# Kernel tuning notes

Measured on AMD Instinct MI355X. Metric: run time of the kernel, lower is better.

The kernel has to match this reference:

```python
import jax, jax.numpy as jnp
import numpy as np

K = 32  # neighbors per query point


def _gather_points(x, idx):
    # x: [B, N, D], idx: [B, M, k] -> [B, M, k, D]
    B, M, k = idx.shape
    D = x.shape[-1]
    flat = jnp.take_along_axis(x, idx.reshape(B, M * k, 1), axis=1)
    return flat.reshape(B, M, k, D)


def setup_inputs() -> dict:
    key = jax.random.key(0)
    k1, k2, k3, k4, k5 = jax.random.split(key, 5)
    B, N, M, Cin = 16, 4096, 1024, 64
    pos = jax.random.normal(k1, (B, N, 3), dtype=jnp.float32)
    features = jax.random.normal(k2, (B, N, Cin), dtype=jnp.float32)
    idx = jax.random.randint(k3, (B, M), 0, N, dtype=jnp.int64)
    # 1x1 conv2d MLP params: (Cin+3) -> 64 -> 128 (use_xyz adds 3 channels)
    W1 = jax.random.normal(k4, (Cin + 3, 64), dtype=jnp.float32) * (1.0 / np.sqrt(Cin + 3))
    b1 = jnp.zeros((64,), dtype=jnp.float32)
    W2 = jax.random.normal(k5, (64, 128), dtype=jnp.float32) * (1.0 / np.sqrt(64))
    b2 = jnp.zeros((128,), dtype=jnp.float32)
    return {"pos": pos, "features": features, "W1": W1, "b1": b1,
            "W2": W2, "b2": b2, "idx": idx}


def reference(pos, features, W1, b1, W2, b2, idx):
    # pos: [B,N,3], features: [B,N,C], idx: [B,M] query-point indices
    pos_q = jnp.take_along_axis(pos, idx[..., None], axis=1)  # [B,M,3]
    # squared-distance knn: [B,M,N]
    d2 = (jnp.sum(pos_q ** 2, -1, keepdims=True)
          + jnp.sum(pos ** 2, -1)[:, None, :]
          - 2.0 * jnp.einsum("bmd,bnd->bmn", pos_q, pos))
    _, nn_idx = jax.lax.top_k(-d2, K)  # [B,M,K] nearest neighbors
    grouped_pos = _gather_points(pos, nn_idx)          # [B,M,K,3]
    grouped_feat = _gather_points(features, nn_idx)    # [B,M,K,C]
    rel = grouped_pos - pos_q[:, :, None, :]           # recenter groups
    x = jnp.concatenate([rel, grouped_feat], axis=-1)  # [B,M,K,C+3] (use_xyz)
    # 1x1 conv2d MLP == per-point linear + ReLU on channel dim
    h = jax.nn.relu(jnp.einsum("bmkc,cd->bmkd", x, W1) + b1)
    h = jax.nn.relu(jnp.einsum("bmkc,cd->bmkd", h, W2) + b2)
    out = jnp.max(h, axis=-2)  # max over K neighbors -> [B,M,128]
    return (pos_q, out)
```

## Files before the change

### kernel.cpp

```cpp
#include <hip/hip_runtime.h>

#define NPTS  4096
#define MQ    1024
#define BATCH 16
#define KNN   32
#define CIN   64
#define H1D   64
#define H2D   128

typedef _Float16 half8 __attribute__((ext_vector_type(8)));
typedef float    floatx4 __attribute__((ext_vector_type(4)));

#define WS_NN_BYTES ((size_t)BATCH * MQ * KNN * 4)
#define W1F_HALVES  (3 * 4 * 64 * 8)
#define W2F_HALVES  (2 * 8 * 64 * 8)
#define WS_P4_OFF   (WS_NN_BYTES + (W1F_HALVES + W2F_HALVES) * 2)

__global__ __launch_bounds__(256) void wprep_kernel(
    const float* __restrict__ W1, const float* __restrict__ W2,
    const float* __restrict__ pos,
    _Float16* __restrict__ wout, float4* __restrict__ pos4)
{
    const int gid = blockIdx.x * 256 + threadIdx.x;
    if (gid < 768) {
        const int s = gid;
        const int kc = s >> 8, nt = (s >> 6) & 3, lane = s & 63;
        const int col = lane & 15, quad = lane >> 4;
        half8 ph;
#pragma unroll
        for (int j = 0; j < 8; ++j) {
            const int k = kc * 32 + quad * 8 + j;
            ph[j] = (k < 67) ? (_Float16)W1[k * H1D + nt * 16 + col] : (_Float16)0.0f;
        }
        *(half8*)(wout + (size_t)s * 8) = ph;
    } else if (gid < 1792) {
        const int s2 = gid - 768;
        const int kc2 = s2 >> 9, nt2 = (s2 >> 6) & 7, lane = s2 & 63;
        const int col = lane & 15, quad = lane >> 4;
        half8 ph;
#pragma unroll
        for (int j = 0; j < 8; ++j) {
            const int k = kc2 * 32 + quad * 8 + j;
            ph[j] = (_Float16)W2[k * H2D + nt2 * 16 + col];
        }
        *(half8*)(wout + (size_t)W1F_HALVES + (size_t)s2 * 8) = ph;
    } else {
        const int p = gid - 1792;
        if (p < BATCH * NPTS) {
            const float px = pos[p * 3 + 0], py = pos[p * 3 + 1], pz = pos[p * 3 + 2];
            float4 v;
            v.x = px; v.y = py; v.z = pz;
            v.w = __fadd_rn(__fadd_rn(__fmul_rn(px, px), __fmul_rn(py, py)),
                            __fmul_rn(pz, pz));
            pos4[p] = v;
        }
    }
}

__global__ __launch_bounds__(256, 4) void knn_kernel(
    const float4* __restrict__ pos4, const int* __restrict__ idx,
    float* __restrict__ pos_q, int* __restrict__ nn)
{
    const int bid = blockIdx.x;
    const int b   = bid >> 10;
    const int m   = bid & (MQ - 1);
    const int t   = threadIdx.x;
    const int wv  = t >> 6, lane = t & 63;

    __shared__ unsigned int hist[2048];
    __shared__ unsigned int wsum[4];
    __shared__ unsigned int sc[8];
    __shared__ unsigned int ckey[64];
    __shared__ int          cidx[64];
    __shared__ int          outidx[KNN];

    const float4* pb4 = pos4 + (size_t)b * NPTS;
    const int qn = idx[(size_t)b * MQ + m];
    const float4 qv = pb4[qn];
    const float qq = qv.w;

#pragma unroll
    for (int j = 0; j < 8; ++j) hist[t + 256 * j] = 0u;
    __syncthreads();

    float4 p[16];
#pragma unroll
    for (int i = 0; i < 16; ++i) p[i] = pb4[i * 256 + t];

    unsigned int k[16];
#pragma unroll
    for (int i = 0; i < 16; ++i) {
        const float qp = __fadd_rn(__fadd_rn(__fmul_rn(qv.x, p[i].x), __fmul_rn(qv.y, p[i].y)),
                                   __fmul_rn(qv.z, p[i].z));
        const float d2 = __fsub_rn(__fadd_rn(qq, p[i].w), __fmul_rn(2.0f, qp));
        unsigned int u = __float_as_uint(d2);
        u = (u & 0x80000000u) ? ~u : (u | 0x80000000u);
        k[i] = u;
        atomicAdd(&hist[u >> 21], 1u);
    }
    __syncthreads();

    unsigned int prefix = 0u, rank = KNN - 1;
    int shift = 21, bcnt;
    for (int level = 0; level < 3; ++level) {
        const int nb = (level < 2) ? 11 : 10;
        const int g  = (1 << nb) >> 8;
        unsigned int cnt[8];
        unsigned int s = 0;
        for (int j = 0; j < g; ++j) { cnt[j] = hist[t * g + j]; s += cnt[j]; }
        unsigned int v = s;
#pragma unroll
        for (int off = 1; off < 64; off <<= 1) {
            const unsigned int o = __shfl_up(v, off);
            if (lane >= off) v += o;
        }
        if (lane == 63) wsum[wv] = v;
        __syncthreads();
        unsigned int woff = 0;
        for (int i = 0; i < wv; ++i) woff += wsum[i];
        const unsigned int incl = woff + v, excl = incl - s;
        if (rank >= excl && rank < incl) {
            unsigned int e = excl;
            for (int j = 0; j < g; ++j) {
                if (rank < e + cnt[j]) {
                    sc[0] = (prefix << nb) | (unsigned int)(t * g + j);
                    sc[1] = rank - e;
                    sc[2] = cnt[j];
                    break;
                }
                e += cnt[j];
            }
        }
        __syncthreads();
        prefix = sc[0];
        rank   = sc[1];
        bcnt   = (int)sc[2];
        if (level == 2 || bcnt <= 64) break;

        const int nshift = (level == 0) ? 10 : 0;
        const int nnb    = (level == 0) ? 11 : 10;
        const unsigned int nmask = (1u << nnb) - 1u;
        __syncthreads();
#pragma unroll
        for (int j = 0; j < 8; ++j) hist[t + 256 * j] = 0u;
        __syncthreads();
#pragma unroll
        for (int i = 0; i < 16; ++i) {
            const unsigned int u = k[i];
            if ((u >> (nshift + nnb)) == prefix)
                atomicAdd(&hist[(u >> nshift) & nmask], 1u);
        }
        shift = nshift;
        __syncthreads();
    }

    if (t == 0) { sc[3] = 0u; sc[4] = 0u; }
    __syncthreads();
#pragma unroll
    for (int i = 0; i < 16; ++i) {
        const unsigned int u = k[i];
        const unsigned int hp = (shift == 0) ? u : (u >> shift);
        if (hp < prefix) {
            outidx[atomicAdd(&sc[3], 1u)] = i * 256 + t;
        } else if (hp == prefix) {
            const unsigned int slot = atomicAdd(&sc[4], 1u);
            if (slot < 64u) { ckey[slot] = u; cidx[slot] = i * 256 + t; }
        }
    }
    __syncthreads();
    const int defcnt  = (int)sc[3];
    const int candcnt = min((int)sc[4], 64);

    if (wv == 0) {
        const unsigned int k_l = (lane < candcnt) ? ckey[lane] : 0xFFFFFFFFu;
        const int          i_l = (lane < candcnt) ? cidx[lane] : 0x7FFFFFFF;
        int rk = 0;
        for (int j = 0; j < candcnt; ++j) {
            const unsigned int kj = __shfl(k_l, j);
            const int          ij = __shfl(i_l, j);
            if (kj < k_l || (kj == k_l && ij < i_l)) ++rk;
        }
        if (lane < candcnt && rk <= (int)rank) outidx[defcnt + rk] = i_l;
    }
    __syncthreads();
    if (t < KNN) nn[(size_t)bid * KNN + t] = outidx[t];
    if (t == 0) {
        pos_q[(size_t)bid * 3 + 0] = qv.x;
        pos_q[(size_t)bid * 3 + 1] = qv.y;
        pos_q[(size_t)bid * 3 + 2] = qv.z;
    }
}

__global__ __launch_bounds__(256, 4) void mlp_kernel(
    const float4* __restrict__ pos4, const float* __restrict__ feat,
    const float* __restrict__ b1, const float* __restrict__ b2,
    const float* __restrict__ pos_q, const int* __restrict__ nn,
    const _Float16* __restrict__ wf, float* __restrict__ out)
{
    __shared__ _Float16 sh[4 * 3072];
    const int t = threadIdx.x;
    const int w = t >> 6, lane = t & 63;
    const int col = lane & 15, quad = lane >> 4;
    const int q = blockIdx.x * 4 + w;
    const int b = q >> 10;
    const int wbase = w * 3072;

    {
        const int r = t >> 1, h = t & 1;
        const int kk = r & 31;
        const int n = nn[(size_t)q * KNN + kk];
        const float4 pv = pos4[(size_t)b * NPTS + n];
        const float4* f4 = (const float4*)(feat + ((size_t)b * NPTS + n) * CIN);
        const int mt = kk >> 4, lrow = kk & 15;
        if (h == 0) {
            float4 ff[12];
#pragma unroll
            for (int ii = 0; ii < 12; ++ii) ff[ii] = f4[ii];
            float rel[3];
            rel[0] = pv.x - pos_q[(size_t)q * 3 + 0];
            rel[1] = pv.y - pos_q[(size_t)q * 3 + 1];
            rel[2] = pv.z - pos_q[(size_t)q * 3 + 2];
#pragma unroll
            for (int ci = 0; ci < 6; ++ci) {
                half8 ph;
#pragma unroll
                for (int jj = 0; jj < 8; ++jj) {
                    const int c = ci * 8 + jj;
                    float v;
                    if (c < 3) v = rel[c];
                    else {
                        const int fc = c - 3;
                        const float4 vv = ff[fc >> 2];
                        v = ((fc & 3) == 0) ? vv.x : ((fc & 3) == 1) ? vv.y
                          : ((fc & 3) == 2) ? vv.z : vv.w;
                    }
                    ph[jj] = (_Float16)v;
                }
                const int kc = ci >> 2, qd = ci & 3;
                *(half8*)&sh[wbase + ((kc * 2 + mt) * 64 + qd * 16 + lrow) * 8] = ph;
            }
        } else {
            float4 ff[5];
#pragma unroll
            for (int ii = 0; ii < 5; ++ii) ff[ii] = f4[11 + ii];
#pragma unroll
            for (int ci = 6; ci < 12; ++ci) {
                half8 ph;
#pragma unroll
                for (int jj = 0; jj < 8; ++jj) {
                    const int c = ci * 8 + jj;
                    float v = 0.0f;
                    if (c < 67) {
                        const int fc = c - 3;
                        const float4 vv = ff[(fc >> 2) - 11];
                        v = ((fc & 3) == 0) ? vv.x : ((fc & 3) == 1) ? vv.y
                          : ((fc & 3) == 2) ? vv.z : vv.w;
                    }
                    ph[jj] = (_Float16)v;
                }
                const int kc = ci >> 2, qd = ci & 3;
                *(half8*)&sh[wbase + ((kc * 2 + mt) * 64 + qd * 16 + lrow) * 8] = ph;
            }
        }
    }

    half8 af[3][2];
#pragma unroll
    for (int kc = 0; kc < 3; ++kc)
#pragma unroll
        for (int mt = 0; mt < 2; ++mt)
            af[kc][mt] = *(const half8*)&sh[wbase + ((kc * 2 + mt) * 64 + lane) * 8];

    half8 w1f[3][4];
#pragma unroll
    for (int kc = 0; kc < 3; ++kc)
#pragma unroll
        for (int nt = 0; nt < 4; ++nt)
            w1f[kc][nt] = *(const half8*)(wf + (size_t)((kc * 4 + nt) * 64 + lane) * 8);

#pragma unroll
    for (int nt = 0; nt < 4; ++nt) {
        const float bv = b1[nt * 16 + col];
        floatx4 acc0 = {bv, bv, bv, bv}, acc1 = acc0;
#pragma unroll
        for (int kc = 0; kc < 3; ++kc) {
            acc0 = __builtin_amdgcn_mfma_f32_16x16x32_f16(af[kc][0], w1f[kc][nt], acc0, 0, 0, 0);
            acc1 = __builtin_amdgcn_mfma_f32_16x16x32_f16(af[kc][1], w1f[kc][nt], acc1, 0, 0, 0);
        }
        const int kc2 = nt >> 1;
        const int quad2 = (((nt & 1) * 16) + col) >> 3;
        const int j2 = col & 7;
#pragma unroll
        for (int mt = 0; mt < 2; ++mt) {
            const floatx4 a = mt ? acc1 : acc0;
#pragma unroll
            for (int reg = 0; reg < 4; ++reg) {
                const int row = quad * 4 + reg;
                sh[wbase + ((kc2 * 2 + mt) * 64 + quad2 * 16 + row) * 8 + j2] =
                    (_Float16)fmaxf(a[reg], 0.0f);
            }
        }
    }

    half8 a2[2][2];
#pragma unroll
    for (int kc2 = 0; kc2 < 2; ++kc2)
#pragma unroll
        for (int mt = 0; mt < 2; ++mt)
            a2[kc2][mt] = *(const half8*)&sh[wbase + ((kc2 * 2 + mt) * 64 + lane) * 8];

    half8 w2f[2][8];
#pragma unroll
    for (int kc2 = 0; kc2 < 2; ++kc2)
#pragma unroll
        for (int nt2 = 0; nt2 < 8; ++nt2)
            w2f[kc2][nt2] = *(const half8*)(wf + (size_t)W1F_HALVES
                                            + (size_t)((kc2 * 8 + nt2) * 64 + lane) * 8);

    float* oq = out + (size_t)q * H2D;
#pragma unroll
    for (int nt2 = 0; nt2 < 8; ++nt2) {
        const float bv = b2[nt2 * 16 + col];
        floatx4 acc0 = {bv, bv, bv, bv}, acc1 = acc0;
#pragma unroll
        for (int kc2 = 0; kc2 < 2; ++kc2) {
            acc0 = __builtin_amdgcn_mfma_f32_16x16x32_f16(a2[kc2][0], w2f[kc2][nt2], acc0, 0, 0, 0);
            acc1 = __builtin_amdgcn_mfma_f32_16x16x32_f16(a2[kc2][1], w2f[kc2][nt2], acc1, 0, 0, 0);
        }
        float mm = fmaxf(fmaxf(fmaxf(acc0[0], acc0[1]), fmaxf(acc0[2], acc0[3])),
                         fmaxf(fmaxf(acc1[0], acc1[1]), fmaxf(acc1[2], acc1[3])));
        mm = fmaxf(mm, 0.0f);
        mm = fmaxf(mm, __shfl_xor(mm, 16));
        mm = fmaxf(mm, __shfl_xor(mm, 32));
        if (lane < 16) oq[nt2 * 16 + lane] = mm;
    }
}

extern "C" void kernel_launch(void* const* d_in, const int* in_sizes, int n_in,
                              void* d_out, int out_size, void* d_ws, size_t ws_size,
                              hipStream_t stream)
{
    const float* pos  = (const float*)d_in[0];
    const float* feat = (const float*)d_in[1];
    const float* W1   = (const float*)d_in[2];
    const float* b1   = (const float*)d_in[3];
    const float* W2   = (const float*)d_in[4];
    const float* b2   = (const float*)d_in[5];
    const int*   idx  = (const int*)d_in[6];

    float* pos_q = (float*)d_out;
    float* out   = (float*)d_out + (size_t)BATCH * MQ * 3;
    int*      nn = (int*)d_ws;
    _Float16* wf = (_Float16*)((char*)d_ws + WS_NN_BYTES);
    float4*   p4 = (float4*)((char*)d_ws + WS_P4_OFF);

    const int prep_threads = 1792 + BATCH * NPTS;
    wprep_kernel<<<(prep_threads + 255) / 256, 256, 0, stream>>>(W1, W2, pos, wf, p4);
    knn_kernel<<<BATCH * MQ, 256, 0, stream>>>(p4, idx, pos_q, nn);
    mlp_kernel<<<BATCH * MQ / 4, 256, 0, stream>>>(p4, feat, b1, b2,
                                                   pos_q, nn, wf, out);
}
```

Measured before the change: 196.4 us.

## Fuse kNN radix-select and MLP into one kernel handling four queries per block

Merges the kNN selection and MLP kernels into a single kernel where each 256-thread block processes four queries. Each position is loaded once and scored against four queries, with per-query histograms in shared memory that is later reused as MLP staging. Neighbour indices stay in LDS instead of a global round trip. Features are optionally pre-converted to fp16 in the prep kernel when workspace allows, halving gather bytes. The cost is more registers per thread (64 keys) and refinement levels serialized per query behind block-wide barriers.

```diff
diff --git a/kernel.cpp b/kernel.cpp
--- a/kernel.cpp
+++ b/kernel.cpp
@@ -11,15 +11,18 @@
 typedef _Float16 half8 __attribute__((ext_vector_type(8)));
 typedef float    floatx4 __attribute__((ext_vector_type(4)));
 
-#define WS_NN_BYTES ((size_t)BATCH * MQ * KNN * 4)
 #define W1F_HALVES  (3 * 4 * 64 * 8)
 #define W2F_HALVES  (2 * 8 * 64 * 8)
-#define WS_P4_OFF   (WS_NN_BYTES + (W1F_HALVES + W2F_HALVES) * 2)
+#define WS_WF_BYTES ((size_t)(W1F_HALVES + W2F_HALVES) * 2)
+#define WS_P4_OFF   WS_WF_BYTES
+#define WS_F16_OFF  (WS_P4_OFF + (size_t)BATCH * NPTS * 16)
+#define WS_NEED     (WS_F16_OFF + (size_t)BATCH * NPTS * CIN * 2)
 
 __global__ __launch_bounds__(256) void wprep_kernel(
     const float* __restrict__ W1, const float* __restrict__ W2,
-    const float* __restrict__ pos,
-    _Float16* __restrict__ wout, float4* __restrict__ pos4)
+    const float* __restrict__ pos, const float* __restrict__ feat,
+    _Float16* __restrict__ wout, float4* __restrict__ pos4,
+    _Float16* __restrict__ feat16, int do_f16)
 {
     const int gid = blockIdx.x * 256 + threadIdx.x;
     if (gid < 768) {
@@ -44,225 +47,334 @@
             ph[j] = (_Float16)W2[k * H2D + nt2 * 16 + col];
         }
         *(half8*)(wout + (size_t)W1F_HALVES + (size_t)s2 * 8) = ph;
-    } else {
+    } else if (gid < 1792 + BATCH * NPTS) {
         const int p = gid - 1792;
-        if (p < BATCH * NPTS) {
-            const float px = pos[p * 3 + 0], py = pos[p * 3 + 1], pz = pos[p * 3 + 2];
-            float4 v;
-            v.x = px; v.y = py; v.z = pz;
-            v.w = __fadd_rn(__fadd_rn(__fmul_rn(px, px), __fmul_rn(py, py)),
-                            __fmul_rn(pz, pz));
-            pos4[p] = v;
+        const float px = pos[p * 3 + 0], py = pos[p * 3 + 1], pz = pos[p * 3 + 2];
+        float4 v;
+        v.x = px; v.y = py; v.z = pz;
+        v.w = __fadd_rn(__fadd_rn(__fmul_rn(px, px), __fmul_rn(py, py)),
+                        __fmul_rn(pz, pz));
+        pos4[p] = v;
+    } else if (do_f16) {
+        const int s = gid - (1792 + BATCH * NPTS);
+        if (s < BATCH * NPTS * 8) {
+            const int row = s >> 3, c8 = (s & 7) * 8;
+            const float4* fp = (const float4*)(feat + (size_t)row * CIN + c8);
+            const float4 a = fp[0], c = fp[1];
+            half8 h;
+            h[0] = (_Float16)a.x; h[1] = (_Float16)a.y;
+            h[2] = (_Float16)a.z; h[3] = (_Float16)a.w;
+            h[4] = (_Float16)c.x; h[5] = (_Float16)c.y;
+            h[6] = (_Float16)c.z; h[7] = (_Float16)c.w;
+            *(half8*)(feat16 + (size_t)row * CIN + c8) = h;
         }
     }
 }
 
-__global__ __launch_bounds__(256, 4) void knn_kernel(
-    const float4* __restrict__ pos4, const int* __restrict__ idx,
-    float* __restrict__ pos_q, int* __restrict__ nn)
+template<int USE_F16>
+__global__ __launch_bounds__(256, 4) void fused_kernel(
+    const float4* __restrict__ pos4, const float* __restrict__ feat,
+    const _Float16* __restrict__ feat16, const int* __restrict__ idx,
+    const float* __restrict__ b1, const float* __restrict__ b2,
+    const _Float16* __restrict__ wf,
+    float* __restrict__ pos_q, float* __restrict__ out)
 {
-    const int bid = blockIdx.x;
-    const int b   = bid >> 10;
-    const int m   = bid & (MQ - 1);
-    const int t   = threadIdx.x;
-    const int wv  = t >> 6, lane = t & 63;
-
-    __shared__ unsigned int hist[2048];
-    __shared__ unsigned int wsum[4];
-    __shared__ unsigned int sc[8];
-    __shared__ unsigned int ckey[64];
-    __shared__ int          cidx[64];
-    __shared__ int          outidx[KNN];
-
+    __shared__ unsigned int histS[4 * 2048];
+    __shared__ unsigned int ckeyS[4][64];
+    __shared__ int          cidxS[4][64];
+    __shared__ int          nnLDS[4][KNN];
+    __shared__ unsigned int scS[4][8];
+    __shared__ unsigned int wsumS[4][4];
+    _Float16* sh = (_Float16*)histS;
+
+    const int t = threadIdx.x;
+    const int w = t >> 6, lane = t & 63;
+    const int qblk = blockIdx.x * 4;
+    const int b = qblk >> 10;
     const float4* pb4 = pos4 + (size_t)b * NPTS;
-    const int qn = idx[(size_t)b * MQ + m];
-    const float4 qv = pb4[qn];
-    const float qq = qv.w;
-
-#pragma unroll
-    for (int j = 0; j < 8; ++j) hist[t + 256 * j] = 0u;
-    __syncthreads();
-
-    float4 p[16];
-#pragma unroll
-    for (int i = 0; i < 16; ++i) p[i] = pb4[i * 256 + t];
-
-    unsigned int k[16];
-#pragma unroll
-    for (int i = 0; i < 16; ++i) {
-        const float qp = __fadd_rn(__fadd_rn(__fmul_rn(qv.x, p[i].x), __fmul_rn(qv.y, p[i].y)),
-                                   __fmul_rn(qv.z, p[i].z));
-        const float d2 = __fsub_rn(__fadd_rn(qq, p[i].w), __fmul_rn(2.0f, qp));
-        unsigned int u = __float_as_uint(d2);
-        u = (u & 0x80000000u) ? ~u : (u | 0x80000000u);
-        k[i] = u;
-        atomicAdd(&hist[u >> 21], 1u);
-    }
-    __syncthreads();
-
-    unsigned int prefix = 0u, rank = KNN - 1;
-    int shift = 21, bcnt;
-    for (int level = 0; level < 3; ++level) {
-        const int nb = (level < 2) ? 11 : 10;
-        const int g  = (1 << nb) >> 8;
-        unsigned int cnt[8];
+
+    float4 qvv[4];
+#pragma unroll
+    for (int qi = 0; qi < 4; ++qi)
+        qvv[qi] = pb4[idx[(size_t)b * MQ + ((qblk & (MQ - 1)) + qi)]];
+
+    {
+        int4* hz = (int4*)histS;
+        const int4 z = make_int4(0, 0, 0, 0);
+#pragma unroll
+        for (int j = 0; j < 8; ++j) hz[t + 256 * j] = z;
+    }
+    __syncthreads();
+
+    unsigned int k[4][16];
+    {
+        float4 pr[4];
+#pragma unroll
+        for (int i = 0; i < 4; ++i) pr[i] = pb4[i * 256 + t];
+#pragma unroll
+        for (int i = 0; i < 16; ++i) {
+            const float4 p = pr[i & 3];
+            if (i < 12) pr[i & 3] = pb4[(i + 4) * 256 + t];
+#pragma unroll
+            for (int qi = 0; qi < 4; ++qi) {
+                const float qp = __fadd_rn(__fadd_rn(__fmul_rn(qvv[qi].x, p.x),
+                                                     __fmul_rn(qvv[qi].y, p.y)),
+                                           __fmul_rn(qvv[qi].z, p.z));
+                const float d2 = __fsub_rn(__fadd_rn(qvv[qi].w, p.w),
+                                           __fmul_rn(2.0f, qp));
+                unsigned int u = __float_as_uint(d2);
+                u = (u & 0x80000000u) ? ~u : (u | 0x80000000u);
+                k[qi][i] = u;
+                atomicAdd(&histS[(qi << 11) | (u >> 21)], 1u);
+            }
+        }
+    }
+    __syncthreads();
+
+    unsigned int sq[4], vq[4];
+#pragma unroll
+    for (int qi = 0; qi < 4; ++qi) {
         unsigned int s = 0;
-        for (int j = 0; j < g; ++j) { cnt[j] = hist[t * g + j]; s += cnt[j]; }
+#pragma unroll
+        for (int j = 0; j < 8; ++j) s += histS[(qi << 11) + t * 8 + j];
         unsigned int v = s;
 #pragma unroll
         for (int off = 1; off < 64; off <<= 1) {
             const unsigned int o = __shfl_up(v, off);
             if (lane >= off) v += o;
         }
-        if (lane == 63) wsum[wv] = v;
-        __syncthreads();
+        if (lane == 63) wsumS[qi][w] = v;
+        sq[qi] = s; vq[qi] = v;
+    }
+    __syncthreads();
+#pragma unroll
+    for (int qi = 0; qi < 4; ++qi) {
         unsigned int woff = 0;
-        for (int i = 0; i < wv; ++i) woff += wsum[i];
-        const unsigned int incl = woff + v, excl = incl - s;
-        if (rank >= excl && rank < incl) {
+#pragma unroll
+        for (int i = 0; i < 4; ++i) if (i < w) woff += wsumS[qi][i];
+        const unsigned int incl = woff + vq[qi], excl = incl - sq[qi];
+        const unsigned int rank0 = KNN - 1;
+        if (rank0 >= excl && rank0 < incl) {
             unsigned int e = excl;
-            for (int j = 0; j < g; ++j) {
-                if (rank < e + cnt[j]) {
-                    sc[0] = (prefix << nb) | (unsigned int)(t * g + j);
-                    sc[1] = rank - e;
-                    sc[2] = cnt[j];
+            for (int j = 0; j < 8; ++j) {
+                const unsigned int c = histS[(qi << 11) + t * 8 + j];
+                if (rank0 < e + c) {
+                    scS[qi][0] = (unsigned int)(t * 8 + j);
+                    scS[qi][1] = rank0 - e;
+                    scS[qi][2] = c;
                     break;
                 }
-                e += cnt[j];
-            }
-        }
-        __syncthreads();
-        prefix = sc[0];
-        rank   = sc[1];
-        bcnt   = (int)sc[2];
-        if (level == 2 || bcnt <= 64) break;
-
-        const int nshift = (level == 0) ? 10 : 0;
-        const int nnb    = (level == 0) ? 11 : 10;
-        const unsigned int nmask = (1u << nnb) - 1u;
-        __syncthreads();
-#pragma unroll
-        for (int j = 0; j < 8; ++j) hist[t + 256 * j] = 0u;
-        __syncthreads();
-#pragma unroll
-        for (int i = 0; i < 16; ++i) {
-            const unsigned int u = k[i];
-            if ((u >> (nshift + nnb)) == prefix)
-                atomicAdd(&hist[(u >> nshift) & nmask], 1u);
-        }
-        shift = nshift;
-        __syncthreads();
-    }
-
-    if (t == 0) { sc[3] = 0u; sc[4] = 0u; }
+                e += c;
+            }
+        }
+    }
+    __syncthreads();
+
+    unsigned int prefq[4], rankq[4]; int shiftq[4];
+#pragma unroll
+    for (int qi = 0; qi < 4; ++qi) {
+        prefq[qi] = scS[qi][0];
+        rankq[qi] = scS[qi][1];
+        shiftq[qi] = 21;
+    }
+
+#pragma unroll
+    for (int qi = 0; qi < 4; ++qi) {
+        if (scS[qi][2] > 64) {
+            for (int lvl = 1; lvl < 3; ++lvl) {
+                const int nb  = (lvl == 1) ? 11 : 10;
+                const int sh2 = (lvl == 1) ? 10 : 0;
+                const unsigned int msk = (1u << nb) - 1u;
+                const int g = (1 << nb) >> 8;
+                for (int j = 0; j < g; ++j) histS[(qi << 11) + t * g + j] = 0u;
+                __syncthreads();
+#pragma unroll
+                for (int i = 0; i < 16; ++i) {
+                    const unsigned int u = k[qi][i];
+                    if ((u >> (sh2 + nb)) == prefq[qi])
+                        atomicAdd(&histS[(qi << 11) + ((u >> sh2) & msk)], 1u);
+                }
+                __syncthreads();
+                unsigned int cnt[8];
+                unsigned int s = 0;
+                for (int j = 0; j < g; ++j) { cnt[j] = histS[(qi << 11) + t * g + j]; s += cnt[j]; }
+                unsigned int v = s;
+#pragma unroll
+                for (int off = 1; off < 64; off <<= 1) {
+                    const unsigned int o = __shfl_up(v, off);
+                    if (lane >= off) v += o;
+                }
+                if (lane == 63) wsumS[qi][w] = v;
+                __syncthreads();
+                unsigned int woff = 0;
+#pragma unroll
+                for (int i2 = 0; i2 < 4; ++i2) if (i2 < w) woff += wsumS[qi][i2];
+                const unsigned int incl = woff + v, excl = incl - s;
+                const unsigned int r = rankq[qi];
+                if (r >= excl && r < incl) {
+                    unsigned int e = excl;
+                    for (int j = 0; j < g; ++j) {
+                        if (r < e + cnt[j]) {
+                            scS[qi][0] = (prefq[qi] << nb) | (unsigned int)(t * g + j);
+                            scS[qi][1] = r - e;
+                            scS[qi][2] = cnt[j];
+                            break;
+                        }
+                        e += cnt[j];
+                    }
+                }
+                __syncthreads();
+                prefq[qi] = scS[qi][0];
+                rankq[qi] = scS[qi][1];
+                shiftq[qi] = sh2;
+                if (scS[qi][2] <= 64u || lvl == 2) break;
+            }
+        }
+    }
+
+    if (t < 4) { scS[t][3] = 0u; scS[t][4] = 0u; }
     __syncthreads();
 #pragma unroll
     for (int i = 0; i < 16; ++i) {
-        const unsigned int u = k[i];
-        const unsigned int hp = (shift == 0) ? u : (u >> shift);
-        if (hp < prefix) {
-            outidx[atomicAdd(&sc[3], 1u)] = i * 256 + t;
-        } else if (hp == prefix) {
-            const unsigned int slot = atomicAdd(&sc[4], 1u);
-            if (slot < 64u) { ckey[slot] = u; cidx[slot] = i * 256 + t; }
-        }
-    }
-    __syncthreads();
-    const int defcnt  = (int)sc[3];
-    const int candcnt = min((int)sc[4], 64);
-
-    if (wv == 0) {
-        const unsigned int k_l = (lane < candcnt) ? ckey[lane] : 0xFFFFFFFFu;
-        const int          i_l = (lane < candcnt) ? cidx[lane] : 0x7FFFFFFF;
+        const int n = i * 256 + t;
+#pragma unroll
+        for (int qi = 0; qi < 4; ++qi) {
+            const unsigned int u = k[qi][i];
+            const unsigned int hp = u >> shiftq[qi];
+            if (hp < prefq[qi]) {
+                const unsigned int slot = atomicAdd(&scS[qi][3], 1u);
+                if (slot < KNN) nnLDS[qi][slot] = n;
+            } else if (hp == prefq[qi]) {
+                const unsigned int slot = atomicAdd(&scS[qi][4], 1u);
+                if (slot < 64u) { ckeyS[qi][slot] = u; cidxS[qi][slot] = n; }
+            }
+        }
+    }
+    __syncthreads();
+
+    {
+        const int candcnt = min((int)scS[w][4], 64);
+        const int defcnt  = min((int)scS[w][3], KNN);
+        const int rnk     = (int)scS[w][1];
+        const unsigned int k_l = (lane < candcnt) ? ckeyS[w][lane] : 0xFFFFFFFFu;
+        const int          i_l = (lane < candcnt) ? cidxS[w][lane] : 0x7FFFFFFF;
         int rk = 0;
         for (int j = 0; j < candcnt; ++j) {
             const unsigned int kj = __shfl(k_l, j);
             const int          ij = __shfl(i_l, j);
             if (kj < k_l || (kj == k_l && ij < i_l)) ++rk;
         }
-        if (lane < candcnt && rk <= (int)rank) outidx[defcnt + rk] = i_l;
-    }
-    __syncthreads();
-    if (t < KNN) nn[(size_t)bid * KNN + t] = outidx[t];
-    if (t == 0) {
-        pos_q[(size_t)bid * 3 + 0] = qv.x;
-        pos_q[(size_t)bid * 3 + 1] = qv.y;
-        pos_q[(size_t)bid * 3 + 2] = qv.z;
-    }
-}
-
-__global__ __launch_bounds__(256, 4) void mlp_kernel(
-    const float4* __restrict__ pos4, const float* __restrict__ feat,
-    const float* __restrict__ b1, const float* __restrict__ b2,
-    const float* __restrict__ pos_q, const int* __restrict__ nn,
-    const _Float16* __restrict__ wf, float* __restrict__ out)
-{
-    __shared__ _Float16 sh[4 * 3072];
-    const int t = threadIdx.x;
-    const int w = t >> 6, lane = t & 63;
-    const int col = lane & 15, quad = lane >> 4;
-    const int q = blockIdx.x * 4 + w;
-    const int b = q >> 10;
+        if (lane < candcnt && rk <= rnk && defcnt + rk < KNN)
+            nnLDS[w][defcnt + rk] = i_l;
+    }
+    if (t < 4) {
+        const float4 qv = (t == 0) ? qvv[0] : (t == 1) ? qvv[1] : (t == 2) ? qvv[2] : qvv[3];
+        pos_q[(size_t)(qblk + t) * 3 + 0] = qv.x;
+        pos_q[(size_t)(qblk + t) * 3 + 1] = qv.y;
+        pos_q[(size_t)(qblk + t) * 3 + 2] = qv.z;
+    }
+    __syncthreads();
+
+    const int q = qblk + w;
     const int wbase = w * 3072;
+    const float4 qme = (w == 0) ? qvv[0] : (w == 1) ? qvv[1] : (w == 2) ? qvv[2] : qvv[3];
 
     {
         const int r = t >> 1, h = t & 1;
         const int kk = r & 31;
-        const int n = nn[(size_t)q * KNN + kk];
-        const float4 pv = pos4[(size_t)b * NPTS + n];
-        const float4* f4 = (const float4*)(feat + ((size_t)b * NPTS + n) * CIN);
+        const int n = nnLDS[w][kk];
         const int mt = kk >> 4, lrow = kk & 15;
-        if (h == 0) {
-            float4 ff[12];
-#pragma unroll
-            for (int ii = 0; ii < 12; ++ii) ff[ii] = f4[ii];
-            float rel[3];
-            rel[0] = pv.x - pos_q[(size_t)q * 3 + 0];
-            rel[1] = pv.y - pos_q[(size_t)q * 3 + 1];
-            rel[2] = pv.z - pos_q[(size_t)q * 3 + 2];
-#pragma unroll
-            for (int ci = 0; ci < 6; ++ci) {
-                half8 ph;
-#pragma unroll
-                for (int jj = 0; jj < 8; ++jj) {
-                    const int c = ci * 8 + jj;
-                    float v;
-                    if (c < 3) v = rel[c];
-                    else {
-                        const int fc = c - 3;
-                        const float4 vv = ff[fc >> 2];
-                        v = ((fc & 3) == 0) ? vv.x : ((fc & 3) == 1) ? vv.y
-                          : ((fc & 3) == 2) ? vv.z : vv.w;
+        if (USE_F16) {
+            const _Float16* frow = feat16 + ((size_t)b * NPTS + n) * CIN;
+            if (h == 0) {
+                const float4 pv = pos4[(size_t)b * NPTS + n];
+                half8 fa[6];
+#pragma unroll
+                for (int ii = 0; ii < 6; ++ii) fa[ii] = *(const half8*)(frow + ii * 8);
+                float relf[3] = {pv.x - qme.x, pv.y - qme.y, pv.z - qme.z};
+#pragma unroll
+                for (int ci = 0; ci < 6; ++ci) {
+                    half8 ph;
+#pragma unroll
+                    for (int jj = 0; jj < 8; ++jj) {
+                        const int c = ci * 8 + jj;
+                        ph[jj] = (c < 3) ? (_Float16)relf[c] : fa[(c - 3) >> 3][(c - 3) & 7];
                     }
-                    ph[jj] = (_Float16)v;
-                }
-                const int kc = ci >> 2, qd = ci & 3;
-                *(half8*)&sh[wbase + ((kc * 2 + mt) * 64 + qd * 16 + lrow) * 8] = ph;
+                    const int kc = ci >> 2, qd = ci & 3;
+                    *(half8*)&sh[wbase + ((kc * 2 + mt) * 64 + qd * 16 + lrow) * 8] = ph;
+                }
+            } else {
+                half8 fb[3];
+#pragma unroll
+                for (int ii = 0; ii < 3; ++ii) fb[ii] = *(const half8*)(frow + 40 + ii * 8);
+#pragma unroll
+                for (int ci = 6; ci < 12; ++ci) {
+                    half8 ph;
+#pragma unroll
+                    for (int jj = 0; jj < 8; ++jj) {
+                        const int c = ci * 8 + jj;
+                        _Float16 v = (_Float16)0.0f;
+                        if (c < 67) { const int f = c - 43; v = fb[f >> 3][f & 7]; }
+                        ph[jj] = v;
+                    }
+                    const int kc = ci >> 2, qd = ci & 3;
+                    *(half8*)&sh[wbase + ((kc * 2 + mt) * 64 + qd * 16 + lrow) * 8] = ph;
+                }
             }
         } else {
-            float4 ff[5];
-#pragma unroll
-            for (int ii = 0; ii < 5; ++ii) ff[ii] = f4[11 + ii];
-#pragma unroll
-            for (int ci = 6; ci < 12; ++ci) {
-                half8 ph;
-#pragma unroll
-                for (int jj = 0; jj < 8; ++jj) {
-                    const int c = ci * 8 + jj;
-                    float v = 0.0f;
-                    if (c < 67) {
-                        const int fc = c - 3;
-                        const float4 vv = ff[(fc >> 2) - 11];
-                        v = ((fc & 3) == 0) ? vv.x : ((fc & 3) == 1) ? vv.y
-                          : ((fc & 3) == 2) ? vv.z : vv.w;
+            const float4* f4 = (const float4*)(feat + ((size_t)b * NPTS + n) * CIN);
+            if (h == 0) {
+                const float4 pv = pos4[(size_t)b * NPTS + n];
+                float4 ff[12];
+#pragma unroll
+                for (int ii = 0; ii < 12; ++ii) ff[ii] = f4[ii];
+                float relf[3] = {pv.x - qme.x, pv.y - qme.y, pv.z - qme.z};
+#pragma unroll
+                for (int ci = 0; ci < 6; ++ci) {
+                    half8 ph;
+#pragma unroll
+                    for (int jj = 0; jj < 8; ++jj) {
+                        const int c = ci * 8 + jj;
+                        float v;
+                        if (c < 3) v = relf[c];
+                        else {
+                            const int fc = c - 3;
+                            const float4 vv = ff[fc >> 2];
+                            v = ((fc & 3) == 0) ? vv.x : ((fc & 3) == 1) ? vv.y
+                              : ((fc & 3) == 2) ? vv.z : vv.w;
+                        }
+                        ph[jj] = (_Float16)v;
                     }
-                    ph[jj] = (_Float16)v;
-                }
-                const int kc = ci >> 2, qd = ci & 3;
-                *(half8*)&sh[wbase + ((kc * 2 + mt) * 64 + qd * 16 + lrow) * 8] = ph;
-            }
-        }
-    }
+                    const int kc = ci >> 2, qd = ci & 3;
+                    *(half8*)&sh[wbase + ((kc * 2 + mt) * 64 + qd * 16 + lrow) * 8] = ph;
+                }
+            } else {
+                float4 ff[5];
+#pragma unroll
+                for (int ii = 0; ii < 5; ++ii) ff[ii] = f4[11 + ii];
+#pragma unroll
+                for (int ci = 6; ci < 12; ++ci) {
+                    half8 ph;
+#pragma unroll
+                    for (int jj = 0; jj < 8; ++jj) {
+                        const int c = ci * 8 + jj;
+                        float v = 0.0f;
+                        if (c < 67) {
+                            const int fc = c - 3;
+                            const float4 vv = ff[(fc >> 2) - 11];
+                            v = ((fc & 3) == 0) ? vv.x : ((fc & 3) == 1) ? vv.y
+                              : ((fc & 3) == 2) ? vv.z : vv.w;
+                        }
+                        ph[jj] = (_Float16)v;
+                    }
+                    const int kc = ci >> 2, qd = ci & 3;
+                    *(half8*)&sh[wbase + ((kc * 2 + mt) * 64 + qd * 16 + lrow) * 8] = ph;
+                }
+            }
+        }
+    }
+
+    const int col = lane & 15, quad = lane >> 4;
 
     half8 af[3][2];
 #pragma unroll
@@ -350,13 +462,18 @@
 
     float* pos_q = (float*)d_out;
     float* out   = (float*)d_out + (size_t)BATCH * MQ * 3;
-    int*      nn = (int*)d_ws;
-    _Float16* wf = (_Float16*)((char*)d_ws + WS_NN_BYTES);
-    float4*   p4 = (float4*)((char*)d_ws + WS_P4_OFF);
-
-    const int prep_threads = 1792 + BATCH * NPTS;
-    wprep_kernel<<<(prep_threads + 255) / 256, 256, 0, stream>>>(W1, W2, pos, wf, p4);
-    knn_kernel<<<BATCH * MQ, 256, 0, stream>>>(p4, idx, pos_q, nn);
-    mlp_kernel<<<BATCH * MQ / 4, 256, 0, stream>>>(p4, feat, b1, b2,
-                                                   pos_q, nn, wf, out);
+    _Float16* wf  = (_Float16*)d_ws;
+    float4*   p4  = (float4*)((char*)d_ws + WS_P4_OFF);
+    _Float16* f16 = (_Float16*)((char*)d_ws + WS_F16_OFF);
+
+    const int use_f16 = (ws_size >= WS_NEED) ? 1 : 0;
+    const int prep_threads = 1792 + BATCH * NPTS + (use_f16 ? BATCH * NPTS * 8 : 0);
+    wprep_kernel<<<(prep_threads + 255) / 256, 256, 0, stream>>>(
+        W1, W2, pos, feat, wf, p4, f16, use_f16);
+    if (use_f16)
+        fused_kernel<1><<<BATCH * MQ / 4, 256, 0, stream>>>(
+            p4, feat, f16, idx, b1, b2, wf, pos_q, out);
+    else
+        fused_kernel<0><<<BATCH * MQ / 4, 256, 0, stream>>>(
+            p4, feat, f16, idx, b1, b2, wf, pos_q, out);
 }
```

After: 200.5 us. 2.1% more time.
